# Kernel tuning notes

Hardware: AMD Instinct MI355X
Metric: run time of the kernel (lower is better)

The kernel has to match this reference:

```python
import jax, jax.numpy as jnp
import numpy as np

QMAX = 255.0  # bit=8 unsigned activation range


def ste_round(x):
    # straight-through round: exact integer rounding in fwd, identity grad
    return x + jax.lax.stop_gradient(jnp.round(x) - x)


def conv3x3(x, w, stride=1):
    return jax.lax.conv_general_dilated(
        x, w, window_strides=(stride, stride), padding=((1, 1), (1, 1)),
        dimension_numbers=('NCHW', 'OIHW', 'NCHW'))


def setup_inputs() -> dict:
    key = jax.random.key(0)
    k0, k1, k2 = jax.random.split(key, 3)
    N, C, H, W = 64, 256, 28, 28
    # uint8 activations and int8 (symmetric) weights, stored as integer-valued fp32
    x = jax.random.randint(k0, (N, C, H, W), 0, 256).astype(jnp.float32)
    w1 = jax.random.randint(k1, (C, C, 3, 3), -128, 128).astype(jnp.float32)
    w2 = jax.random.randint(k2, (C, C, 3, 3), -128, 128).astype(jnp.float32)
    f = jnp.float32
    return dict(
        x=x, w1=w1, w2=w2,
        s_x=f(0.05), z_x=f(128.0),
        s_w1=f(0.01), s_conv1=f(0.08), z_conv1=f(120.0),
        s_w2=f(0.01), s_conv2=f(0.07), z_conv2=f(130.0),
        s_add=f(0.09), z_add=f(125.0))


def qconv(x_q, w_q, s_in, z_in, s_w, s_out, z_out, stride=1):
    # integer-arithmetic conv: sum((x - z_in) * w) then requantize
    acc = conv3x3(x_q - z_in, w_q, stride)
    M = s_in * s_w / s_out  # per-cluster requant multiplier (cluster 0)
    return jnp.clip(ste_round(M * acc) + z_out, 0.0, QMAX)


def qadd(a, s_a, z_a, b, s_b, z_b, s_out, z_out):
    # fused dequant of both branches + residual add + requant
    y = (s_a / s_out) * (a - z_a) + (s_b / s_out) * (b - z_b)
    return jnp.clip(ste_round(y) + z_out, 0.0, QMAX)


def reference(x, w1, w2, s_x, z_x, s_w1, s_conv1, z_conv1,
              s_w2, s_conv2, z_conv2, s_add, z_add):
    out = qconv(x, w1, s_x, z_x, s_w1, s_conv1, z_conv1)          # conv1
    out = qconv(out, w2, s_conv1, z_conv1, s_w2, s_conv2, z_conv2)  # conv2
    return qadd(x, s_x, z_x, out, s_conv2, z_conv2, s_add, z_add)   # shortcut
```

## Files before the change

### kernel.cpp

```cpp
#include <hip/hip_runtime.h>
#include <stdint.h>

#define HWP 784
#define NPOS 50176

typedef int int4v  __attribute__((ext_vector_type(4)));
typedef int int16v __attribute__((ext_vector_type(16)));
using as1_cv = const __attribute__((address_space(1))) void;
using as3_v  = __attribute__((address_space(3))) void;

__global__ __launch_bounds__(256) void k_x_to_nhwc(const float* __restrict__ x,
                                                   int8_t* __restrict__ x8) {
    __shared__ __align__(16) int8_t tile[64][116];
    int b = blockIdx.x;
    int ct = b & 3;
    int hwt = (b >> 2) % 7;
    int n = b / 28;
    int c0 = ct * 64, hw0 = hwt * 112;
    int tid = threadIdx.x;
#pragma unroll
    for (int k = 0; k < 28; ++k) {
        int e = tid + k * 256;
        int c = e / 112, hh = e % 112;
        float v = x[((size_t)(n * 256 + c0 + c)) * HWP + hw0 + hh];
        tile[c][hh] = (int8_t)((int)v - 128);
    }
    __syncthreads();
    int cc = tid & 63;
    int pb = tid >> 6;
#pragma unroll
    for (int j = 0; j < 28; ++j) {
        int pi = pb + j * 4;
        x8[((size_t)(n * HWP + hw0 + pi)) * 256 + c0 + cc] = tile[cc][pi];
    }
}

__global__ __launch_bounds__(256) void k_w_prep(const float* __restrict__ w,
                                                int8_t* __restrict__ w8,
                                                int* __restrict__ wsum) {
    __shared__ int red[256];
    const int oc = blockIdx.x;
    const int t = threadIdx.x;
    const float* src = w + (size_t)oc * 2304 + (size_t)t * 9;
    const int g = oc >> 5;
    const int l = ((t >> 4) & 1) * 32 + (oc & 31);
    const int j = t & 15;
    const int s2 = (t >> 5) & 1;
    const int kb = t >> 6;
    int acc = 0;
#pragma unroll
    for (int tap = 0; tap < 9; ++tap) {
        int wv = (int)src[tap];
        acc += wv;
        int oo = ((((tap * 4 + kb) * 2 + s2) * 8 + g) * 64 + l) * 16 + j;
        w8[oo] = (int8_t)wv;
    }
    red[t] = acc;
    __syncthreads();
    for (int st = 128; st > 0; st >>= 1) {
        if (t < st) red[t] += red[t + st];
        __syncthreads();
    }
    if (t == 0) wsum[oc] = red[0];
}

template<bool FUSED>
__global__ __launch_bounds__(256) void k_qconv_t(const int8_t* __restrict__ in8,
        const int8_t* __restrict__ w8, const int* __restrict__ wsum,
        const float* __restrict__ s_in_p, const float* __restrict__ s_w_p,
        const float* __restrict__ s_out_p, const float* __restrict__ z_in_p,
        const float* __restrict__ z_out_p, int8_t* __restrict__ out8,
        const int8_t* __restrict__ x8, const float* __restrict__ sxp,
        const float* __restrict__ zxp, const float* __restrict__ sap,
        const float* __restrict__ zap, float* __restrict__ outf) {
    __shared__ __align__(16) int8_t slab[81920];
    const int tid = threadIdx.x;
    const int lane = tid & 63;
    const int half = lane >> 5;
    const int wv = tid >> 6;
    const int p0 = blockIdx.x * 256;
    const int g = blockIdx.y;

    {
        const int base_byte = (p0 - 29) * 256;
        const int maxb = NPOS * 256 - 16;
#pragma unroll
        for (int i = 0; i < 20; ++i) {
            int chunkid = tid + i * 256;
            int q = chunkid >> 4;
            int cslot = chunkid & 15;
            int gchunk = cslot ^ (q & 15);
            int src = base_byte + q * 256 + gchunk * 16;
            src = src < 0 ? 0 : (src > maxb ? maxb : src);
            __builtin_amdgcn_global_load_lds((as1_cv*)(in8 + src),
                                             (as3_v*)&slab[chunkid * 16], 16, 0, 0);
        }
    }

    int rowpos[2], ph[2], pw[2];
#pragma unroll
    for (int mt = 0; mt < 2; ++mt) {
        rowpos[mt] = wv * 64 + mt * 32 + (lane & 31);
        int p = p0 + rowpos[mt];
        int hw = p % HWP;
        ph[mt] = hw / 28;
        pw[mt] = hw % 28;
    }

    const int zi = (int)z_in_p[0] - 128;
    const int spl = (zi & 0xff) * 0x01010101;
    int4v pad;
    pad[0] = spl; pad[1] = spl; pad[2] = spl; pad[3] = spl;

    int16v acc[2][2];
#pragma unroll
    for (int mt = 0; mt < 2; ++mt)
#pragma unroll
        for (int nt = 0; nt < 2; ++nt)
#pragma unroll
            for (int r = 0; r < 16; ++r) acc[mt][nt][r] = 0;

    const int8_t* wlane = w8 + g * 2048 + lane * 16;
    auto loadB = [&](int u, int4v* b0, int4v* b1) {
        const int8_t* wb = wlane + (size_t)u * 16384;
        b0[0] = *(const int4v*)(wb);
        b0[1] = *(const int4v*)(wb + 1024);
        b1[0] = *(const int4v*)(wb + 8192);
        b1[1] = *(const int4v*)(wb + 9216);
    };

    int4v cb0[2], cb1[2];
    loadB(0, cb0, cb1);

    __syncthreads();

#pragma unroll 1
    for (int tap = 0; tap < 9; ++tap) {
        const int dh = tap / 3 - 1;
        const int dw = tap % 3 - 1;
        int qbase[2];
        bool okm[2];
#pragma unroll
        for (int mt = 0; mt < 2; ++mt) {
            qbase[mt] = rowpos[mt] + dh * 28 + dw + 29;
            okm[mt] = ((unsigned)(ph[mt] + dh) < 28u) & ((unsigned)(pw[mt] + dw) < 28u);
        }
#pragma unroll
        for (int kb = 0; kb < 4; ++kb) {
            const int u = tap * 4 + kb;
            int4v nb0[2], nb1[2];
            int un = u < 35 ? u + 1 : 35;
            loadB(un, nb0, nb1);
            int4v a0[2], a1[2];
#pragma unroll
            for (int mt = 0; mt < 2; ++mt) {
                int q = qbase[mt];
                int sw = q & 15;
                int base = q * 256;
                int4v v0 = *(const int4v*)&slab[base + ((kb * 4 + half) ^ sw) * 16];
                int4v v1 = *(const int4v*)&slab[base + ((kb * 4 + 2 + half) ^ sw) * 16];
                a0[mt] = okm[mt] ? v0 : pad;
                a1[mt] = okm[mt] ? v1 : pad;
            }
#pragma unroll
            for (int mt = 0; mt < 2; ++mt)
#pragma unroll
                for (int nt = 0; nt < 2; ++nt) {
                    acc[mt][nt] = __builtin_amdgcn_mfma_i32_32x32x32_i8(a0[mt], cb0[nt], acc[mt][nt], 0, 0, 0);
                    acc[mt][nt] = __builtin_amdgcn_mfma_i32_32x32x32_i8(a1[mt], cb1[nt], acc[mt][nt], 0, 0, 0);
                }
#pragma unroll
            for (int nt = 0; nt < 2; ++nt) { cb0[nt] = nb0[nt]; cb1[nt] = nb1[nt]; }
        }
    }

    const float Mf = s_in_p[0] * s_w_p[0] / s_out_p[0];
    const float zof = z_out_p[0];
    const int zoffi = 128 - (int)z_in_p[0];

    if (!FUSED) {
#pragma unroll
        for (int nt = 0; nt < 2; ++nt) {
            int oc = g * 64 + nt * 32 + (lane & 31);
            int corr = zoffi * wsum[oc];
#pragma unroll
            for (int mt = 0; mt < 2; ++mt) {
#pragma unroll
                for (int r = 0; r < 16; ++r) {
                    int row = (r & 3) + 8 * (r >> 2) + 4 * half;
                    int pos = p0 + wv * 64 + mt * 32 + row;
                    float q = rintf(Mf * (float)(acc[mt][nt][r] + corr)) + zof;
                    q = fminf(fmaxf(q, 0.0f), 255.0f);
                    out8[(size_t)pos * 256 + oc] = (int8_t)((int)q - 128);
                }
            }
        }
    } else {
        const float ra = sxp[0] / sap[0];
        const float rb = s_out_p[0] / sap[0];
        const float zx = zxp[0];
        const float z2 = z_out_p[0];
        const float za = zap[0];
        __syncthreads();
        float* tp = (float*)(slab + wv * 16640);
#pragma unroll
        for (int nt = 0; nt < 2; ++nt) {
            int ocl = nt * 32 + (lane & 31);
            int oc = g * 64 + ocl;
            int corr = zoffi * wsum[oc];
#pragma unroll
            for (int mt = 0; mt < 2; ++mt) {
#pragma unroll
                for (int r = 0; r < 16; ++r) {
                    int row = (r & 3) + 8 * (r >> 2) + 4 * half;
                    int pl = mt * 32 + row;
                    int pos = p0 + wv * 64 + pl;
                    float q2 = rintf(Mf * (float)(acc[mt][nt][r] + corr)) + zof;
                    q2 = fminf(fmaxf(q2, 0.0f), 255.0f);
                    float av = (float)((int)x8[(size_t)pos * 256 + oc] + 128) - zx;
                    float bv = q2 - z2;
                    float y = ra * av + rb * bv;
                    float qf = rintf(y) + za;
                    qf = fminf(fmaxf(qf, 0.0f), 255.0f);
                    tp[pl * 65 + ocl] = qf;
                }
            }
        }
        int p = p0 + wv * 64 + lane;
        int n = p / HWP;
        int hw = p % HWP;
        float* obase = outf + (size_t)n * (256 * HWP) + hw + (size_t)(g * 64) * HWP;
#pragma unroll 8
        for (int oc = 0; oc < 64; ++oc) {
            obase[(size_t)oc * HWP] = tp[lane * 65 + oc];
        }
    }
}

extern "C" void kernel_launch(void* const* d_in, const int* in_sizes, int n_in,
                              void* d_out, int out_size, void* d_ws, size_t ws_size,
                              hipStream_t stream) {
    (void)in_sizes; (void)n_in; (void)out_size; (void)ws_size;
    const float* x    = (const float*)d_in[0];
    const float* w1   = (const float*)d_in[1];
    const float* w2   = (const float*)d_in[2];
    const float* s_x  = (const float*)d_in[3];
    const float* z_x  = (const float*)d_in[4];
    const float* s_w1 = (const float*)d_in[5];
    const float* s_c1 = (const float*)d_in[6];
    const float* z_c1 = (const float*)d_in[7];
    const float* s_w2 = (const float*)d_in[8];
    const float* s_c2 = (const float*)d_in[9];
    const float* z_c2 = (const float*)d_in[10];
    const float* s_ad = (const float*)d_in[11];
    const float* z_ad = (const float*)d_in[12];
    float* out = (float*)d_out;

    int8_t* ws   = (int8_t*)d_ws;
    int8_t* x8   = ws;
    int8_t* o1   = ws + 12845056;
    int8_t* w8a  = ws + 25690112;
    int8_t* w8b  = ws + 26279936;
    int*    wsum1 = (int*)(ws + 26869760);
    int*    wsum2 = (int*)(ws + 26870784);

    k_x_to_nhwc<<<1792, 256, 0, stream>>>(x, x8);
    k_w_prep<<<256, 256, 0, stream>>>(w1, w8a, wsum1);
    k_w_prep<<<256, 256, 0, stream>>>(w2, w8b, wsum2);
    k_qconv_t<false><<<dim3(196, 4), 256, 0, stream>>>(x8, w8a, wsum1,
        s_x, s_w1, s_c1, z_x, z_c1, o1,
        nullptr, nullptr, nullptr, nullptr, nullptr, nullptr);
    k_qconv_t<true><<<dim3(196, 4), 256, 0, stream>>>(o1, w8b, wsum2,
        s_c1, s_w2, s_c2, z_c1, z_c2, nullptr,
        x8, s_x, z_x, s_ad, z_ad, out);
}
```

Measured before the change: 216.9 us.

## Use channel-group planar int8 layout, halve conv tile, vectorize transpose and epilogue

Activation storage changes from plain NHWC to four channel-group planes of 64 channels each, so every conv block reads and writes contiguous 64-byte rows for its output group. The conv tile drops to 128 positions per block with one M-tile per wave, which cuts LDS use so three blocks can fit per CU and doubles the grid. The input transpose kernel now uses float4 loads and packs bytes into 16-byte stores, and the fused epilogue reads the residual with vectorized loads. The cost is less weight reuse per block and more redundant halo loading per position.

```diff
diff --git a/kernel.cpp b/kernel.cpp
--- a/kernel.cpp
+++ b/kernel.cpp
@@ -3,35 +3,63 @@
 
 #define HWP 784
 #define NPOS 50176
-
-typedef int int4v  __attribute__((ext_vector_type(4)));
-typedef int int16v __attribute__((ext_vector_type(16)));
+#define PLN ((size_t)NPOS * 64)
+
+typedef int   int4v   __attribute__((ext_vector_type(4)));
+typedef int   int16v  __attribute__((ext_vector_type(16)));
+typedef float float4v __attribute__((ext_vector_type(4)));
 using as1_cv = const __attribute__((address_space(1))) void;
 using as3_v  = __attribute__((address_space(3))) void;
 
-__global__ __launch_bounds__(256) void k_x_to_nhwc(const float* __restrict__ x,
-                                                   int8_t* __restrict__ x8) {
-    __shared__ __align__(16) int8_t tile[64][116];
-    int b = blockIdx.x;
-    int ct = b & 3;
-    int hwt = (b >> 2) % 7;
-    int n = b / 28;
-    int c0 = ct * 64, hw0 = hwt * 112;
-    int tid = threadIdx.x;
-#pragma unroll
-    for (int k = 0; k < 28; ++k) {
+__global__ __launch_bounds__(256) void k_nhwc(const float* __restrict__ x,
+                                              int8_t* __restrict__ x8) {
+    __shared__ int lA[256 * 15];
+    __shared__ __align__(16) int lB[56 * 68];
+    const int tid = threadIdx.x;
+    const int P0 = blockIdx.x * 56;
+    const int n = P0 / HWP;
+    const int hw0 = P0 % HWP;
+    const float* xb = x + (size_t)n * 256 * HWP + hw0;
+#pragma unroll
+    for (int k = 0; k < 14; ++k) {
         int e = tid + k * 256;
-        int c = e / 112, hh = e % 112;
-        float v = x[((size_t)(n * 256 + c0 + c)) * HWP + hw0 + hh];
-        tile[c][hh] = (int8_t)((int)v - 128);
-    }
-    __syncthreads();
-    int cc = tid & 63;
-    int pb = tid >> 6;
-#pragma unroll
-    for (int j = 0; j < 28; ++j) {
-        int pi = pb + j * 4;
-        x8[((size_t)(n * HWP + hw0 + pi)) * 256 + c0 + cc] = tile[cc][pi];
+        int c = e / 14, pq = e % 14;
+        float4v v = *(const float4v*)(xb + (size_t)c * HWP + pq * 4);
+        int b0 = ((int)v[0] - 128) & 255;
+        int b1 = ((int)v[1] - 128) & 255;
+        int b2 = ((int)v[2] - 128) & 255;
+        int b3 = ((int)v[3] - 128) & 255;
+        lA[c * 15 + pq] = b0 | (b1 << 8) | (b2 << 16) | (b3 << 24);
+    }
+    __syncthreads();
+#pragma unroll
+    for (int k = 0; k < 4; ++k) {
+        int u = tid + k * 256;
+        if (u < 896) {
+            int cg = u / 14, pq = u % 14;
+            int d0 = lA[(cg * 4 + 0) * 15 + pq];
+            int d1 = lA[(cg * 4 + 1) * 15 + pq];
+            int d2 = lA[(cg * 4 + 2) * 15 + pq];
+            int d3 = lA[(cg * 4 + 3) * 15 + pq];
+#pragma unroll
+            for (int j = 0; j < 4; ++j) {
+                int sh = j * 8;
+                int o = ((d0 >> sh) & 255) | (((d1 >> sh) & 255) << 8)
+                      | (((d2 >> sh) & 255) << 16) | (((d3 >> sh) & 255) << 24);
+                lB[(pq * 4 + j) * 68 + cg] = o;
+            }
+        }
+    }
+    __syncthreads();
+#pragma unroll
+    for (int k = 0; k < 4; ++k) {
+        int ch = tid + k * 256;
+        if (ch < 896) {
+            int g = ch / 224, rem = ch % 224;
+            int pos = rem >> 2, c4 = rem & 3;
+            int4v val = *(const int4v*)&lB[pos * 68 + g * 16 + c4 * 4];
+            *(int4v*)(x8 + (size_t)g * PLN + (size_t)(P0 + pos) * 64 + c4 * 16) = val;
+        }
     }
 }
 
@@ -65,7 +93,7 @@
 }
 
 template<bool FUSED>
-__global__ __launch_bounds__(256) void k_qconv_t(const int8_t* __restrict__ in8,
+__global__ __launch_bounds__(256, 3) void k_qconv_t(const int8_t* __restrict__ in8,
         const int8_t* __restrict__ w8, const int* __restrict__ wsum,
         const float* __restrict__ s_in_p, const float* __restrict__ s_w_p,
         const float* __restrict__ s_out_p, const float* __restrict__ z_in_p,
@@ -73,52 +101,48 @@
         const int8_t* __restrict__ x8, const float* __restrict__ sxp,
         const float* __restrict__ zxp, const float* __restrict__ sap,
         const float* __restrict__ zap, float* __restrict__ outf) {
-    __shared__ __align__(16) int8_t slab[81920];
+    __shared__ __align__(16) int8_t slab[47616];
     const int tid = threadIdx.x;
     const int lane = tid & 63;
     const int half = lane >> 5;
     const int wv = tid >> 6;
-    const int p0 = blockIdx.x * 256;
+    const int p0 = blockIdx.x * 128;
     const int g = blockIdx.y;
 
     {
-        const int base_byte = (p0 - 29) * 256;
-        const int maxb = NPOS * 256 - 16;
-#pragma unroll
-        for (int i = 0; i < 20; ++i) {
-            int chunkid = tid + i * 256;
-            int q = chunkid >> 4;
-            int cslot = chunkid & 15;
-            int gchunk = cslot ^ (q & 15);
-            int src = base_byte + q * 256 + gchunk * 16;
-            src = src < 0 ? 0 : (src > maxb ? maxb : src);
-            __builtin_amdgcn_global_load_lds((as1_cv*)(in8 + src),
-                                             (as3_v*)&slab[chunkid * 16], 16, 0, 0);
-        }
-    }
-
-    int rowpos[2], ph[2], pw[2];
-#pragma unroll
-    for (int mt = 0; mt < 2; ++mt) {
-        rowpos[mt] = wv * 64 + mt * 32 + (lane & 31);
-        int p = p0 + rowpos[mt];
-        int hw = p % HWP;
-        ph[mt] = hw / 28;
-        pw[mt] = hw % 28;
-    }
+#pragma unroll
+        for (int k = 0; k < 12; ++k) {
+            int chunkid = tid + k * 256;
+            if (chunkid < 2976) {
+                int q = chunkid >> 4;
+                int cs = chunkid & 15;
+                int cg = cs ^ (q & 15);
+                int qg = p0 - 29 + q;
+                qg = qg < 0 ? 0 : (qg > NPOS - 1 ? NPOS - 1 : qg);
+                const int8_t* src = in8 + (size_t)(cg >> 2) * PLN
+                                        + (size_t)qg * 64 + (cg & 3) * 16;
+                __builtin_amdgcn_global_load_lds((as1_cv*)src,
+                                                 (as3_v*)&slab[chunkid * 16], 16, 0, 0);
+            }
+        }
+    }
+
+    const int rowpos = wv * 32 + (lane & 31);
+    const int p = p0 + rowpos;
+    const int hwp_ = p % HWP;
+    const int ph = hwp_ / 28;
+    const int pw = hwp_ % 28;
 
     const int zi = (int)z_in_p[0] - 128;
     const int spl = (zi & 0xff) * 0x01010101;
     int4v pad;
     pad[0] = spl; pad[1] = spl; pad[2] = spl; pad[3] = spl;
 
-    int16v acc[2][2];
-#pragma unroll
-    for (int mt = 0; mt < 2; ++mt)
-#pragma unroll
-        for (int nt = 0; nt < 2; ++nt)
-#pragma unroll
-            for (int r = 0; r < 16; ++r) acc[mt][nt][r] = 0;
+    int16v acc[2];
+#pragma unroll
+    for (int nt = 0; nt < 2; ++nt)
+#pragma unroll
+        for (int r = 0; r < 16; ++r) acc[nt][r] = 0;
 
     const int8_t* wlane = w8 + g * 2048 + lane * 16;
     auto loadB = [&](int u, int4v* b0, int4v* b1) {
@@ -128,7 +152,6 @@
         b1[0] = *(const int4v*)(wb + 8192);
         b1[1] = *(const int4v*)(wb + 9216);
     };
-
     int4v cb0[2], cb1[2];
     loadB(0, cb0, cb1);
 
@@ -138,37 +161,25 @@
     for (int tap = 0; tap < 9; ++tap) {
         const int dh = tap / 3 - 1;
         const int dw = tap % 3 - 1;
-        int qbase[2];
-        bool okm[2];
-#pragma unroll
-        for (int mt = 0; mt < 2; ++mt) {
-            qbase[mt] = rowpos[mt] + dh * 28 + dw + 29;
-            okm[mt] = ((unsigned)(ph[mt] + dh) < 28u) & ((unsigned)(pw[mt] + dw) < 28u);
-        }
+        const int qrow = rowpos + dh * 28 + dw + 29;
+        const bool ok = ((unsigned)(ph + dh) < 28u) & ((unsigned)(pw + dw) < 28u);
+        const int sw = qrow & 15;
+        const int base = qrow * 256;
 #pragma unroll
         for (int kb = 0; kb < 4; ++kb) {
             const int u = tap * 4 + kb;
             int4v nb0[2], nb1[2];
             int un = u < 35 ? u + 1 : 35;
             loadB(un, nb0, nb1);
-            int4v a0[2], a1[2];
-#pragma unroll
-            for (int mt = 0; mt < 2; ++mt) {
-                int q = qbase[mt];
-                int sw = q & 15;
-                int base = q * 256;
-                int4v v0 = *(const int4v*)&slab[base + ((kb * 4 + half) ^ sw) * 16];
-                int4v v1 = *(const int4v*)&slab[base + ((kb * 4 + 2 + half) ^ sw) * 16];
-                a0[mt] = okm[mt] ? v0 : pad;
-                a1[mt] = okm[mt] ? v1 : pad;
-            }
-#pragma unroll
-            for (int mt = 0; mt < 2; ++mt)
-#pragma unroll
-                for (int nt = 0; nt < 2; ++nt) {
-                    acc[mt][nt] = __builtin_amdgcn_mfma_i32_32x32x32_i8(a0[mt], cb0[nt], acc[mt][nt], 0, 0, 0);
-                    acc[mt][nt] = __builtin_amdgcn_mfma_i32_32x32x32_i8(a1[mt], cb1[nt], acc[mt][nt], 0, 0, 0);
-                }
+            int4v a0 = *(const int4v*)&slab[base + ((kb * 4 + half) ^ sw) * 16];
+            int4v a1 = *(const int4v*)&slab[base + ((kb * 4 + 2 + half) ^ sw) * 16];
+            a0 = ok ? a0 : pad;
+            a1 = ok ? a1 : pad;
+#pragma unroll
+            for (int nt = 0; nt < 2; ++nt) {
+                acc[nt] = __builtin_amdgcn_mfma_i32_32x32x32_i8(a0, cb0[nt], acc[nt], 0, 0, 0);
+                acc[nt] = __builtin_amdgcn_mfma_i32_32x32x32_i8(a1, cb1[nt], acc[nt], 0, 0, 0);
+            }
 #pragma unroll
             for (int nt = 0; nt < 2; ++nt) { cb0[nt] = nb0[nt]; cb1[nt] = nb1[nt]; }
         }
@@ -179,20 +190,18 @@
     const int zoffi = 128 - (int)z_in_p[0];
 
     if (!FUSED) {
+        int8_t* o8p = out8 + (size_t)g * PLN;
 #pragma unroll
         for (int nt = 0; nt < 2; ++nt) {
             int oc = g * 64 + nt * 32 + (lane & 31);
             int corr = zoffi * wsum[oc];
 #pragma unroll
-            for (int mt = 0; mt < 2; ++mt) {
-#pragma unroll
-                for (int r = 0; r < 16; ++r) {
-                    int row = (r & 3) + 8 * (r >> 2) + 4 * half;
-                    int pos = p0 + wv * 64 + mt * 32 + row;
-                    float q = rintf(Mf * (float)(acc[mt][nt][r] + corr)) + zof;
-                    q = fminf(fmaxf(q, 0.0f), 255.0f);
-                    out8[(size_t)pos * 256 + oc] = (int8_t)((int)q - 128);
-                }
+            for (int r = 0; r < 16; ++r) {
+                int row = (r & 3) + 8 * (r >> 2) + 4 * half;
+                int pos = p0 + wv * 32 + row;
+                float q = rintf(Mf * (float)(acc[nt][r] + corr)) + zof;
+                q = fminf(fmaxf(q, 0.0f), 255.0f);
+                o8p[(size_t)pos * 64 + nt * 32 + (lane & 31)] = (int8_t)((int)q - 128);
             }
         }
     } else {
@@ -202,37 +211,40 @@
         const float z2 = z_out_p[0];
         const float za = zap[0];
         __syncthreads();
-        float* tp = (float*)(slab + wv * 16640);
+        float* tp = (float*)slab + wv * 2080;
 #pragma unroll
         for (int nt = 0; nt < 2; ++nt) {
-            int ocl = nt * 32 + (lane & 31);
-            int oc = g * 64 + ocl;
+            int oc = g * 64 + nt * 32 + (lane & 31);
             int corr = zoffi * wsum[oc];
 #pragma unroll
-            for (int mt = 0; mt < 2; ++mt) {
-#pragma unroll
-                for (int r = 0; r < 16; ++r) {
-                    int row = (r & 3) + 8 * (r >> 2) + 4 * half;
-                    int pl = mt * 32 + row;
-                    int pos = p0 + wv * 64 + pl;
-                    float q2 = rintf(Mf * (float)(acc[mt][nt][r] + corr)) + zof;
-                    q2 = fminf(fmaxf(q2, 0.0f), 255.0f);
-                    float av = (float)((int)x8[(size_t)pos * 256 + oc] + 128) - zx;
-                    float bv = q2 - z2;
-                    float y = ra * av + rb * bv;
-                    float qf = rintf(y) + za;
-                    qf = fminf(fmaxf(qf, 0.0f), 255.0f);
-                    tp[pl * 65 + ocl] = qf;
-                }
-            }
-        }
-        int p = p0 + wv * 64 + lane;
-        int n = p / HWP;
-        int hw = p % HWP;
-        float* obase = outf + (size_t)n * (256 * HWP) + hw + (size_t)(g * 64) * HWP;
-#pragma unroll 8
-        for (int oc = 0; oc < 64; ++oc) {
-            obase[(size_t)oc * HWP] = tp[lane * 65 + oc];
+            for (int r = 0; r < 16; ++r) {
+                int pl = (r & 3) + 8 * (r >> 2) + 4 * half;
+                float q2 = rintf(Mf * (float)(acc[nt][r] + corr)) + zof;
+                q2 = fminf(fmaxf(q2, 0.0f), 255.0f);
+                tp[pl * 65 + nt * 32 + (lane & 31)] = q2;
+            }
+        }
+        const int pl = lane & 31;
+        const int hh = half;
+        const int pglob = p0 + wv * 32 + pl;
+        const int8_t* x8p = x8 + (size_t)g * PLN + (size_t)pglob * 64 + hh * 32;
+        int4v r0 = *(const int4v*)x8p;
+        int4v r1 = *(const int4v*)(x8p + 16);
+        int xb[8];
+        xb[0] = r0[0]; xb[1] = r0[1]; xb[2] = r0[2]; xb[3] = r0[3];
+        xb[4] = r1[0]; xb[5] = r1[1]; xb[6] = r1[2]; xb[7] = r1[3];
+        const int n = pglob / HWP;
+        const int hwo = pglob % HWP;
+        float* obase = outf + ((size_t)(n * 256 + g * 64 + hh * 32)) * HWP + hwo;
+#pragma unroll
+        for (int j = 0; j < 32; ++j) {
+            int bv = (xb[j >> 2] >> ((j & 3) * 8)) & 255;
+            int xval = (int)(int8_t)bv + 128;
+            float q2 = tp[pl * 65 + hh * 32 + j];
+            float y = ra * ((float)xval - zx) + rb * (q2 - z2);
+            float qf = rintf(y) + za;
+            qf = fminf(fmaxf(qf, 0.0f), 255.0f);
+            obase[(size_t)j * HWP] = qf;
         }
     }
 }
@@ -256,21 +268,21 @@
     const float* z_ad = (const float*)d_in[12];
     float* out = (float*)d_out;
 
-    int8_t* ws   = (int8_t*)d_ws;
-    int8_t* x8   = ws;
-    int8_t* o1   = ws + 12845056;
-    int8_t* w8a  = ws + 25690112;
-    int8_t* w8b  = ws + 26279936;
+    int8_t* ws    = (int8_t*)d_ws;
+    int8_t* x8    = ws;
+    int8_t* o1    = ws + 12845056;
+    int8_t* w8a   = ws + 25690112;
+    int8_t* w8b   = ws + 26279936;
     int*    wsum1 = (int*)(ws + 26869760);
     int*    wsum2 = (int*)(ws + 26870784);
 
-    k_x_to_nhwc<<<1792, 256, 0, stream>>>(x, x8);
+    k_nhwc<<<896, 256, 0, stream>>>(x, x8);
     k_w_prep<<<256, 256, 0, stream>>>(w1, w8a, wsum1);
     k_w_prep<<<256, 256, 0, stream>>>(w2, w8b, wsum2);
-    k_qconv_t<false><<<dim3(196, 4), 256, 0, stream>>>(x8, w8a, wsum1,
+    k_qconv_t<false><<<dim3(392, 4), 256, 0, stream>>>(x8, w8a, wsum1,
         s_x, s_w1, s_c1, z_x, z_c1, o1,
         nullptr, nullptr, nullptr, nullptr, nullptr, nullptr);
-    k_qconv_t<true><<<dim3(196, 4), 256, 0, stream>>>(o1, w8b, wsum2,
+    k_qconv_t<true><<<dim3(392, 4), 256, 0, stream>>>(o1, w8b, wsum2,
         s_c1, s_w2, s_c2, z_c1, z_c2, nullptr,
         x8, s_x, z_x, s_ad, z_ad, out);
 }
```

Result: no change. 215.9 us (-0.5%).
